# Kernel tuning notes

Hardware: AMD Instinct MI355X
Metric: run time of the kernel (lower is better)

Reference implementation:

```python
import jax, jax.numpy as jnp
import numpy as np

N_NODES = 50000
N_EDGES = 800000
N_GRAPHS = 2500
IN_DIM = 128
HID = 64
HEADS = 2
NEG_SLOPE = 0.2


def _gat_layer(x, W, att_src, att_dst, bias, src, dst, n):
    # W: [F_in, H*C], att_*: [H, C], bias: [C]
    h = (x @ W).reshape(n, HEADS, HID)            # [N,H,C]
    a_src = jnp.sum(h * att_src[None], axis=-1)   # [N,H]
    a_dst = jnp.sum(h * att_dst[None], axis=-1)   # [N,H]
    e = jax.nn.leaky_relu(a_src[src] + a_dst[dst], NEG_SLOPE)  # [E,H]
    # segment softmax over destination neighborhoods
    m = jax.ops.segment_max(e, dst, num_segments=n)            # [N,H]
    m = jnp.where(jnp.isfinite(m), m, 0.0)
    ex = jnp.exp(e - m[dst])
    s = jax.ops.segment_sum(ex, dst, num_segments=n)           # [N,H]
    alpha = ex / jnp.maximum(s[dst], 1e-16)                    # [E,H]
    msg = h[src] * alpha[:, :, None]                           # [E,H,C]
    out = jax.ops.segment_sum(msg, dst, num_segments=n)        # [N,H,C]
    return out.mean(axis=1) + bias                             # concat=False -> head mean


def _with_self_loops(edge_index, n):
    loop = jnp.arange(n, dtype=edge_index.dtype)
    src = jnp.concatenate([edge_index[0], loop])
    dst = jnp.concatenate([edge_index[1], loop])
    return src, dst


def setup_inputs() -> dict:
    key = jax.random.key(0)
    ks = jax.random.split(key, 16)
    x = jax.random.normal(ks[0], (N_NODES, IN_DIM), dtype=jnp.float32)
    edge_index = jax.random.randint(ks[1], (2, N_EDGES), 0, N_NODES, dtype=jnp.int32)
    batch = jnp.sort(jax.random.randint(ks[2], (N_NODES,), 0, N_GRAPHS, dtype=jnp.int32))

    def glorot(k, shape):
        fan = shape[0] + shape[-1]
        return jax.random.normal(k, shape, dtype=jnp.float32) * np.sqrt(2.0 / fan)

    inp = {"x": x, "edge_index": edge_index, "batch": batch}
    dims = [IN_DIM, HID, HID]
    for i in range(3):
        inp[f"W{i+1}"] = glorot(ks[3 + 4 * i], (dims[i], HEADS * HID))
        inp[f"att_src{i+1}"] = glorot(ks[4 + 4 * i], (HEADS, HID))
        inp[f"att_dst{i+1}"] = glorot(ks[5 + 4 * i], (HEADS, HID))
        inp[f"b{i+1}"] = jnp.zeros((HID,), dtype=jnp.float32)
    inp["lin_w"] = glorot(ks[15], (HID, 1))
    inp["lin_b"] = jnp.zeros((1,), dtype=jnp.float32)
    return inp


def reference(x, W1, att_src1, att_dst1, b1, W2, att_src2, att_dst2, b2,
              W3, att_src3, att_dst3, b3, lin_w, lin_b, edge_index, batch):
    n = x.shape[0]
    src, dst = _with_self_loops(edge_index, n)
    h = jax.nn.relu(_gat_layer(x, W1, att_src1, att_dst1, b1, src, dst, n))
    h = jax.nn.relu(_gat_layer(h, W2, att_src2, att_dst2, b2, src, dst, n))
    h = jax.nn.relu(_gat_layer(h, W3, att_src3, att_dst3, b3, src, dst, n))
    # global mean pool over graphs
    sums = jax.ops.segment_sum(h, batch, num_segments=N_GRAPHS)          # [G,C]
    cnt = jax.ops.segment_sum(jnp.ones((n,), h.dtype), batch, num_segments=N_GRAPHS)
    pooled = sums / jnp.maximum(cnt, 1.0)[:, None]
    return pooled @ lin_w + lin_b                                        # [G,1]
```

## Files before the change

### kernel.cpp

```cpp
#include <hip/hip_runtime.h>
#include <hip/hip_fp16.h>
#include <math.h>


__device__ __forceinline__ float lrelu(float v) { return v > 0.f ? v : 0.2f * v; }

__device__ __forceinline__ float wave_max(float v) {
  for (int off = 32; off; off >>= 1) v = fmaxf(v, __shfl_xor(v, off, 64));
  return v;
}
__device__ __forceinline__ float half_sum(float v) {
  for (int off = 16; off; off >>= 1) v += __shfl_xor(v, off, 64);
  return v;
}
__device__ __forceinline__ float half_max(float v) {
  for (int off = 16; off; off >>= 1) v = fmaxf(v, __shfl_xor(v, off, 64));
  return v;
}

__global__ void count_rank(const int* __restrict__ ei, int* __restrict__ deg,
                           int* __restrict__ rank, int e) {
  int j0 = blockIdx.x * 1024 + threadIdx.x;
#pragma unroll
  for (int k = 0; k < 4; ++k) {
    int j = j0 + k * 256;
    if (j < e) rank[j] = atomicAdd(&deg[ei[e + j]], 1);
  }
}

__global__ void scan_blocks(const int* __restrict__ deg, int* __restrict__ row_ptr,
                            int* __restrict__ btot, int n) {
  __shared__ int sm[256];
  int i = blockIdx.x * 256 + threadIdx.x;
  int v = (i < n) ? deg[i] : 0;
  sm[threadIdx.x] = v;
  __syncthreads();
  for (int off = 1; off < 256; off <<= 1) {
    int t = (threadIdx.x >= off) ? sm[threadIdx.x - off] : 0;
    __syncthreads();
    sm[threadIdx.x] += t;
    __syncthreads();
  }
  if (i < n) row_ptr[i] = sm[threadIdx.x] - v;
  if (threadIdx.x == 255) btot[blockIdx.x] = sm[255];
}

__global__ void scan_totals(int* __restrict__ btot, int nb) {
  __shared__ int sm[256];
  int v = (threadIdx.x < nb) ? btot[threadIdx.x] : 0;
  sm[threadIdx.x] = v;
  __syncthreads();
  for (int off = 1; off < 256; off <<= 1) {
    int t = (threadIdx.x >= off) ? sm[threadIdx.x - off] : 0;
    __syncthreads();
    sm[threadIdx.x] += t;
    __syncthreads();
  }
  if (threadIdx.x < nb) btot[threadIdx.x] = sm[threadIdx.x] - v;
}

__global__ void scan_add(int* __restrict__ row_ptr, int* __restrict__ csr,
                         const int* __restrict__ btot, int n, int total) {
  int i = blockIdx.x * 256 + threadIdx.x;
  if (i < n) {
    int v = row_ptr[i] + btot[blockIdx.x] + i;
    row_ptr[i] = v;
    csr[v] = i;
  }
  if (i == 0) row_ptr[n] = total;
}

__global__ void place_kernel(const int* __restrict__ ei, const int* __restrict__ rank,
                             const int* __restrict__ row_ptr, int* __restrict__ csr,
                             int e) {
  int j0 = blockIdx.x * 1024 + threadIdx.x;
#pragma unroll
  for (int k = 0; k < 4; ++k) {
    int j = j0 + k * 256;
    if (j < e) {
      int d = ei[e + j];
      csr[row_ptr[d] + 1 + rank[j]] = ei[j];
    }
  }
}

template <int K>
__global__ __launch_bounds__(256) void gemm_att(const float* __restrict__ X,
                                                const float* __restrict__ W,
                                                const float* __restrict__ asw,
                                                const float* __restrict__ adw,
                                                __half* __restrict__ H16,
                                                float* __restrict__ a_src,
                                                float* __restrict__ a_dst, int N) {
  __shared__ float Xs[64 * (K + 4)];
  int tid = threadIdx.x;
  int row0 = blockIdx.x * 64;
  int head = blockIdx.y;

  for (int idx = tid; idx < 64 * K; idx += 256) {
    int r = idx / K;
    int k = idx - r * K;
    int gr = row0 + r;
    if (gr >= N) gr = N - 1;
    Xs[r * (K + 4) + k] = X[(size_t)gr * K + k];
  }
  __syncthreads();

  int cgrp = tid & 15;
  int rg = tid >> 4;
  int c0 = head * 64 + cgrp * 4;
  const float* wp = W + c0;
  float acc[4][4] = {};

#pragma unroll 2
  for (int k = 0; k < K; k += 4) {
    float4 xr[4];
#pragma unroll
    for (int j = 0; j < 4; ++j)
      xr[j] = *(const float4*)(&Xs[(rg * 4 + j) * (K + 4) + k]);
#pragma unroll
    for (int kk = 0; kk < 4; ++kk) {
      float4 w4 = *(const float4*)(wp + (k + kk) * 128);
#pragma unroll
      for (int j = 0; j < 4; ++j) {
        float xv = ((const float*)&xr[j])[kk];
        acc[j][0] = fmaf(xv, w4.x, acc[j][0]);
        acc[j][1] = fmaf(xv, w4.y, acc[j][1]);
        acc[j][2] = fmaf(xv, w4.z, acc[j][2]);
        acc[j][3] = fmaf(xv, w4.w, acc[j][3]);
      }
    }
  }

  float4 aw = *(const float4*)(asw + c0);
  float4 dw = *(const float4*)(adw + c0);
#pragma unroll
  for (int j = 0; j < 4; ++j) {
    int r = row0 + rg * 4 + j;
    float sp = acc[j][0] * aw.x + acc[j][1] * aw.y + acc[j][2] * aw.z + acc[j][3] * aw.w;
    float dp = acc[j][0] * dw.x + acc[j][1] * dw.y + acc[j][2] * dw.z + acc[j][3] * dw.w;
#pragma unroll
    for (int off = 1; off < 16; off <<= 1) {
      sp += __shfl_xor(sp, off, 64);
      dp += __shfl_xor(dp, off, 64);
    }
    if (r < N) {
      union { __half2 h2[2]; uint2 u; } pk;
      pk.h2[0] = __floats2half2_rn(acc[j][0], acc[j][1]);
      pk.h2[1] = __floats2half2_rn(acc[j][2], acc[j][3]);
      *(uint2*)(H16 + (size_t)r * 128 + c0) = pk.u;
      if (cgrp == 0) {
        a_src[r * 2 + head] = sp;
        a_dst[r * 2 + head] = dp;
      }
    }
  }
}

__device__ __forceinline__ void ld_grp8(const __half* __restrict__ H16, int half_,
                                        int c8, int headsel, int sub, int s,
                                        float p0, float p1, int g,
                                        uint4* h, float* q) {
#pragma unroll
  for (int k = 0; k < 4; ++k) {
    int idx = half_ + g * 8 + k * 2 + sub;
    int st = __shfl(s, idx, 64);
    float q0 = __shfl(p0, idx, 64);
    float q1 = __shfl(p1, idx, 64);
    q[k] = headsel ? q1 : q0;
    h[k] = *(const uint4*)(H16 + (size_t)st * 128 + c8);
  }
}
__device__ __forceinline__ void fma_grp8(const uint4* h, const float* q,
                                         float* acc) {
#pragma unroll
  for (int k = 0; k < 4; ++k) {
    union { uint u; __half2 h2; } a, b, c, d;
    a.u = h[k].x; b.u = h[k].y; c.u = h[k].z; d.u = h[k].w;
    float2 f0 = __half22float2(a.h2);
    float2 f1 = __half22float2(b.h2);
    float2 f2 = __half22float2(c.h2);
    float2 f3 = __half22float2(d.h2);
    acc[0] = fmaf(f0.x, q[k], acc[0]);
    acc[1] = fmaf(f0.y, q[k], acc[1]);
    acc[2] = fmaf(f1.x, q[k], acc[2]);
    acc[3] = fmaf(f1.y, q[k], acc[3]);
    acc[4] = fmaf(f2.x, q[k], acc[4]);
    acc[5] = fmaf(f2.y, q[k], acc[5]);
    acc[6] = fmaf(f3.x, q[k], acc[6]);
    acc[7] = fmaf(f3.y, q[k], acc[7]);
  }
}
__device__ __forceinline__ void gather_pipe8(const __half* __restrict__ H16, int half_,
                                             int c8, int headsel, int sub, int s,
                                             float p0, float p1, int maxcnt,
                                             float* acc) {
  int groups = (maxcnt + 7) >> 3;
  uint4 ha[4], hb[4];
  float qa[4], qb[4];
  ld_grp8(H16, half_, c8, headsel, sub, s, p0, p1, 0, ha, qa);
  int g = 1;
  for (; g + 1 < groups; g += 2) {
    ld_grp8(H16, half_, c8, headsel, sub, s, p0, p1, g, hb, qb);
    fma_grp8(ha, qa, acc);
    ld_grp8(H16, half_, c8, headsel, sub, s, p0, p1, g + 1, ha, qa);
    fma_grp8(hb, qb, acc);
  }
  if (g < groups) {
    ld_grp8(H16, half_, c8, headsel, sub, s, p0, p1, g, hb, qb);
    fma_grp8(ha, qa, acc);
    fma_grp8(hb, qb, acc);
  } else {
    fma_grp8(ha, qa, acc);
  }
}

template <int POOL>
__global__ __launch_bounds__(256) void aggregate_fused(
    const __half* __restrict__ H16, const float* __restrict__ a_src,
    const float* __restrict__ a_dst, const float* __restrict__ bias,
    const int* __restrict__ row_ptr, const int* __restrict__ csr,
    float* __restrict__ out, const float* __restrict__ lw,
    float* __restrict__ pvn, int N) {
  int lane = threadIdx.x & 63;
  int half_ = lane & 32;
  int l32 = lane & 31;
  int dst = blockIdx.x * 8 + ((threadIdx.x >> 6) << 1) + (half_ >> 5);
  bool live = dst < N;
  int beg = live ? row_ptr[dst] : 0;
  int end = live ? row_ptr[dst + 1] : 0;
  int cnt = end - beg;
  float2 ad = live ? ((const float2*)a_dst)[dst] : make_float2(0.f, 0.f);
  int sub = l32 >> 4;
  int m = l32 & 15;
  int c8 = m * 8;
  int headsel = m >> 3;
  float acc[8] = {};
  float inv0, inv1;

  int maxcnt = (int)wave_max((float)cnt);
  if (maxcnt < 1) maxcnt = 1;

  if (maxcnt <= 32) {
    int j = beg + l32;
    bool valid = l32 < cnt;
    int s = valid ? csr[j] : 0;
    float2 as = ((const float2*)a_src)[s];
    float e0 = valid ? lrelu(as.x + ad.x) : -1e30f;
    float e1 = valid ? lrelu(as.y + ad.y) : -1e30f;
    float m0 = half_max(e0);
    float m1 = half_max(e1);
    float p0 = __expf(e0 - m0);
    float p1 = __expf(e1 - m1);
    inv0 = 1.f / fmaxf(half_sum(valid ? p0 : 0.f), 1e-16f);
    inv1 = 1.f / fmaxf(half_sum(valid ? p1 : 0.f), 1e-16f);
    gather_pipe8(H16, half_, c8, headsel, sub, s, p0, p1, maxcnt, acc);
  } else {
    float m0 = -1e30f, m1 = -1e30f, s0 = 0.f, s1 = 0.f;
    for (int base = 0; base < maxcnt; base += 32) {
      int j = beg + base + l32;
      bool valid = (base + l32) < cnt;
      int s = valid ? csr[j] : 0;
      float2 as = ((const float2*)a_src)[s];
      float e0 = valid ? lrelu(as.x + ad.x) : -1e30f;
      float e1 = valid ? lrelu(as.y + ad.y) : -1e30f;
      float nm0 = fmaxf(m0, half_max(e0));
      float nm1 = fmaxf(m1, half_max(e1));
      s0 = s0 * __expf(m0 - nm0) + half_sum(valid ? __expf(e0 - nm0) : 0.f);
      s1 = s1 * __expf(m1 - nm1) + half_sum(valid ? __expf(e1 - nm1) : 0.f);
      m0 = nm0; m1 = nm1;
    }
    inv0 = 1.f / fmaxf(s0, 1e-16f);
    inv1 = 1.f / fmaxf(s1, 1e-16f);
    for (int base = 0; base < maxcnt; base += 32) {
      int j = beg + base + l32;
      bool valid = (base + l32) < cnt;
      int s = valid ? csr[j] : 0;
      float2 as = ((const float2*)a_src)[s];
      float e0 = valid ? lrelu(as.x + ad.x) : -1e30f;
      float e1 = valid ? lrelu(as.y + ad.y) : -1e30f;
      float p0 = __expf(e0 - m0);
      float p1 = __expf(e1 - m1);
      int rem = maxcnt - base;
      if (rem > 32) rem = 32;
      gather_pipe8(H16, half_, c8, headsel, sub, s, p0, p1, rem, acc);
    }
  }

#pragma unroll
  for (int j = 0; j < 8; ++j) acc[j] += __shfl_xor(acc[j], 16, 64);

  float il = headsel ? inv1 : inv0;
  float v[8], w[8];
#pragma unroll
  for (int j = 0; j < 8; ++j) v[j] = acc[j] * il;
#pragma unroll
  for (int j = 0; j < 8; ++j) w[j] = __shfl_xor(v[j], 8, 64);

  if (m < 8 && sub == 0 && live) {
    int c = m * 8;
    float4 b0 = *(const float4*)(bias + c);
    float4 b1 = *(const float4*)(bias + c + 4);
    float r[8];
    r[0] = fmaxf(0.5f * (v[0] + w[0]) + b0.x, 0.f);
    r[1] = fmaxf(0.5f * (v[1] + w[1]) + b0.y, 0.f);
    r[2] = fmaxf(0.5f * (v[2] + w[2]) + b0.z, 0.f);
    r[3] = fmaxf(0.5f * (v[3] + w[3]) + b0.w, 0.f);
    r[4] = fmaxf(0.5f * (v[4] + w[4]) + b1.x, 0.f);
    r[5] = fmaxf(0.5f * (v[5] + w[5]) + b1.y, 0.f);
    r[6] = fmaxf(0.5f * (v[6] + w[6]) + b1.z, 0.f);
    r[7] = fmaxf(0.5f * (v[7] + w[7]) + b1.w, 0.f);
    if (POOL) {
      float4 l0 = *(const float4*)(lw + c);
      float4 l1 = *(const float4*)(lw + c + 4);
      float pv = r[0] * l0.x + r[1] * l0.y + r[2] * l0.z + r[3] * l0.w +
                 r[4] * l1.x + r[5] * l1.y + r[6] * l1.z + r[7] * l1.w;
      pv += __shfl_xor(pv, 1, 64);
      pv += __shfl_xor(pv, 2, 64);
      pv += __shfl_xor(pv, 4, 64);
      if (m == 0) pvn[dst] = pv;
    } else {
      *(float4*)(out + (size_t)dst * 64 + c) = make_float4(r[0], r[1], r[2], r[3]);
      *(float4*)(out + (size_t)dst * 64 + c + 4) = make_float4(r[4], r[5], r[6], r[7]);
    }
  }
}

__device__ __forceinline__ int lower_bound(const int* __restrict__ a, int n, int key) {
  int lo = 0, hi = n;
  while (lo < hi) {
    int mid = (lo + hi) >> 1;
    if (a[mid] < key) lo = mid + 1; else hi = mid;
  }
  return lo;
}

__global__ void finalize_kernel(const float* __restrict__ pvn,
                                const int* __restrict__ batch,
                                const float* __restrict__ lb,
                                float* __restrict__ out, int N, int G) {
  int g = blockIdx.x * blockDim.x + threadIdx.x;
  if (g >= G) return;
  int lo = lower_bound(batch, N, g);
  int hi = lower_bound(batch, N, g + 1);
  float s = 0.f;
  for (int i = lo; i < hi; ++i) s += pvn[i];
  out[g] = s / fmaxf((float)(hi - lo), 1.f) + lb[0];
}

extern "C" void kernel_launch(void* const* d_in, const int* in_sizes, int n_in,
                              void* d_out, int out_size, void* d_ws, size_t ws_size,
                              hipStream_t stream) {
  const float* x   = (const float*)d_in[0];
  const int* ei    = (const int*)d_in[1];
  const int* batch = (const int*)d_in[2];
  const float* W1  = (const float*)d_in[3];
  const float* as1 = (const float*)d_in[4];
  const float* ad1 = (const float*)d_in[5];
  const float* b1  = (const float*)d_in[6];
  const float* W2  = (const float*)d_in[7];
  const float* as2 = (const float*)d_in[8];
  const float* ad2 = (const float*)d_in[9];
  const float* b2  = (const float*)d_in[10];
  const float* W3  = (const float*)d_in[11];
  const float* as3 = (const float*)d_in[12];
  const float* ad3 = (const float*)d_in[13];
  const float* b3  = (const float*)d_in[14];
  const float* lw  = (const float*)d_in[15];
  const float* lb  = (const float*)d_in[16];
  float* out = (float*)d_out;

  const int N = in_sizes[0] / 128;
  const int E = in_sizes[1] / 2;
  const int ET = N + E;
  const int G = out_size;
  const int NB = (N + 255) / 256;

  char* p = (char*)d_ws;
  auto take = [&](size_t bytes) {
    char* r = p;
    p += (bytes + 255) & ~(size_t)255;
    return r;
  };
  int* deg      = (int*)take((size_t)N * 4);
  int* row_ptr  = (int*)take((size_t)(N + 1) * 4);
  int* rank     = (int*)take((size_t)E * 4);
  int* btot     = (int*)take((size_t)NB * 4);
  int* csr      = (int*)take((size_t)ET * 4);
  __half* H16   = (__half*)take((size_t)N * 128 * 2);
  float* a_src  = (float*)take((size_t)N * 2 * 4);
  float* a_dst  = (float*)take((size_t)N * 2 * 4);
  float* bufA   = (float*)take((size_t)N * 64 * 4);
  float* bufB   = (float*)take((size_t)N * 64 * 4);
  float* pvn    = (float*)take((size_t)N * 4);
  (void)ws_size; (void)n_in;

  hipMemsetAsync(deg, 0, (size_t)N * 4, stream);
  count_rank<<<(E + 1023) / 1024, 256, 0, stream>>>(ei, deg, rank, E);
  scan_blocks<<<NB, 256, 0, stream>>>(deg, row_ptr, btot, N);
  scan_totals<<<1, 256, 0, stream>>>(btot, NB);
  scan_add<<<NB, 256, 0, stream>>>(row_ptr, csr, btot, N, ET);
  place_kernel<<<(E + 1023) / 1024, 256, 0, stream>>>(ei, rank, row_ptr, csr, E);

  const dim3 gblk((N + 63) / 64, 2);
  const int ablk = (N + 7) / 8;

  gemm_att<128><<<gblk, 256, 0, stream>>>(x, W1, as1, ad1, H16, a_src, a_dst, N);
  aggregate_fused<0><<<ablk, 256, 0, stream>>>(H16, a_src, a_dst, b1, row_ptr, csr,
                                               bufA, lw, pvn, N);
  gemm_att<64><<<gblk, 256, 0, stream>>>(bufA, W2, as2, ad2, H16, a_src, a_dst, N);
  aggregate_fused<0><<<ablk, 256, 0, stream>>>(H16, a_src, a_dst, b2, row_ptr, csr,
                                               bufB, lw, pvn, N);
  gemm_att<64><<<gblk, 256, 0, stream>>>(bufB, W3, as3, ad3, H16, a_src, a_dst, N);
  aggregate_fused<1><<<ablk, 256, 0, stream>>>(H16, a_src, a_dst, b3, row_ptr, csr,
                                               bufA, lw, pvn, N);

  finalize_kernel<<<(G + 255) / 256, 256, 0, stream>>>(pvn, batch, lb, out, N, G);
}
```

Measured before the change: 348.4 us.

## Use one wavefront per destination node and K-chunk the GEMM shared tile

The aggregation kernel now maps each destination node to a full 64-lane wavefront instead of a half-wave, with four edge slots of 16 lanes each gathering rows in parallel, and uses wave-wide softmax reductions. This removes the per-wave maxcnt coupling between two nodes and gives more lanes per edge batch, but with about 17 edges per node most lanes are idle in the softmax phase and each wave does less work. Separately, the GEMM now stages X through a fixed 64-column shared tile in K chunks, reducing shared memory for K=128 at the cost of extra synchronisation.

```diff
diff --git a/kernel.cpp b/kernel.cpp
--- a/kernel.cpp
+++ b/kernel.cpp
@@ -9,12 +9,8 @@
   for (int off = 32; off; off >>= 1) v = fmaxf(v, __shfl_xor(v, off, 64));
   return v;
 }
-__device__ __forceinline__ float half_sum(float v) {
-  for (int off = 16; off; off >>= 1) v += __shfl_xor(v, off, 64);
-  return v;
-}
-__device__ __forceinline__ float half_max(float v) {
-  for (int off = 16; off; off >>= 1) v = fmaxf(v, __shfl_xor(v, off, 64));
+__device__ __forceinline__ float wave_sum(float v) {
+  for (int off = 32; off; off >>= 1) v += __shfl_xor(v, off, 64);
   return v;
 }
 
@@ -92,44 +88,46 @@
                                                 __half* __restrict__ H16,
                                                 float* __restrict__ a_src,
                                                 float* __restrict__ a_dst, int N) {
-  __shared__ float Xs[64 * (K + 4)];
+  __shared__ float Xs[64 * 68];
   int tid = threadIdx.x;
   int row0 = blockIdx.x * 64;
   int head = blockIdx.y;
-
-  for (int idx = tid; idx < 64 * K; idx += 256) {
-    int r = idx / K;
-    int k = idx - r * K;
-    int gr = row0 + r;
-    if (gr >= N) gr = N - 1;
-    Xs[r * (K + 4) + k] = X[(size_t)gr * K + k];
-  }
-  __syncthreads();
-
   int cgrp = tid & 15;
   int rg = tid >> 4;
   int c0 = head * 64 + cgrp * 4;
-  const float* wp = W + c0;
   float acc[4][4] = {};
 
+  for (int kc = 0; kc < K; kc += 64) {
+    for (int idx = tid; idx < 64 * 64; idx += 256) {
+      int r = idx >> 6;
+      int k = idx & 63;
+      int gr = row0 + r;
+      if (gr >= N) gr = N - 1;
+      Xs[r * 68 + k] = X[(size_t)gr * K + kc + k];
+    }
+    __syncthreads();
+
+    const float* wp = W + (size_t)kc * 128 + c0;
 #pragma unroll 2
-  for (int k = 0; k < K; k += 4) {
-    float4 xr[4];
-#pragma unroll
-    for (int j = 0; j < 4; ++j)
-      xr[j] = *(const float4*)(&Xs[(rg * 4 + j) * (K + 4) + k]);
-#pragma unroll
-    for (int kk = 0; kk < 4; ++kk) {
-      float4 w4 = *(const float4*)(wp + (k + kk) * 128);
-#pragma unroll
-      for (int j = 0; j < 4; ++j) {
-        float xv = ((const float*)&xr[j])[kk];
-        acc[j][0] = fmaf(xv, w4.x, acc[j][0]);
-        acc[j][1] = fmaf(xv, w4.y, acc[j][1]);
-        acc[j][2] = fmaf(xv, w4.z, acc[j][2]);
-        acc[j][3] = fmaf(xv, w4.w, acc[j][3]);
+    for (int k = 0; k < 64; k += 4) {
+      float4 xr[4];
+#pragma unroll
+      for (int j = 0; j < 4; ++j)
+        xr[j] = *(const float4*)(&Xs[(rg * 4 + j) * 68 + k]);
+#pragma unroll
+      for (int kk = 0; kk < 4; ++kk) {
+        float4 w4 = *(const float4*)(wp + (k + kk) * 128);
+#pragma unroll
+        for (int j = 0; j < 4; ++j) {
+          float xv = ((const float*)&xr[j])[kk];
+          acc[j][0] = fmaf(xv, w4.x, acc[j][0]);
+          acc[j][1] = fmaf(xv, w4.y, acc[j][1]);
+          acc[j][2] = fmaf(xv, w4.z, acc[j][2]);
+          acc[j][3] = fmaf(xv, w4.w, acc[j][3]);
+        }
       }
     }
+    __syncthreads();
   }
 
   float4 aw = *(const float4*)(asw + c0);
@@ -157,61 +155,61 @@
   }
 }
 
-__device__ __forceinline__ void ld_grp8(const __half* __restrict__ H16, int half_,
-                                        int c8, int headsel, int sub, int s,
+__device__ __forceinline__ void ld_grpw(const __half* __restrict__ H16, int q,
+                                        int c8, int headsel, int s,
                                         float p0, float p1, int g,
-                                        uint4* h, float* q) {
-#pragma unroll
-  for (int k = 0; k < 4; ++k) {
-    int idx = half_ + g * 8 + k * 2 + sub;
-    int st = __shfl(s, idx, 64);
-    float q0 = __shfl(p0, idx, 64);
-    float q1 = __shfl(p1, idx, 64);
-    q[k] = headsel ? q1 : q0;
+                                        uint4* h, float* qv) {
+#pragma unroll
+  for (int k = 0; k < 2; ++k) {
+    int e = g * 8 + k * 4 + q;
+    int st = __shfl(s, e, 64);
+    float q0 = __shfl(p0, e, 64);
+    float q1 = __shfl(p1, e, 64);
+    qv[k] = headsel ? q1 : q0;
     h[k] = *(const uint4*)(H16 + (size_t)st * 128 + c8);
   }
 }
-__device__ __forceinline__ void fma_grp8(const uint4* h, const float* q,
+__device__ __forceinline__ void fma_grpw(const uint4* h, const float* qv,
                                          float* acc) {
 #pragma unroll
-  for (int k = 0; k < 4; ++k) {
+  for (int k = 0; k < 2; ++k) {
     union { uint u; __half2 h2; } a, b, c, d;
     a.u = h[k].x; b.u = h[k].y; c.u = h[k].z; d.u = h[k].w;
     float2 f0 = __half22float2(a.h2);
     float2 f1 = __half22float2(b.h2);
     float2 f2 = __half22float2(c.h2);
     float2 f3 = __half22float2(d.h2);
-    acc[0] = fmaf(f0.x, q[k], acc[0]);
-    acc[1] = fmaf(f0.y, q[k], acc[1]);
-    acc[2] = fmaf(f1.x, q[k], acc[2]);
-    acc[3] = fmaf(f1.y, q[k], acc[3]);
-    acc[4] = fmaf(f2.x, q[k], acc[4]);
-    acc[5] = fmaf(f2.y, q[k], acc[5]);
-    acc[6] = fmaf(f3.x, q[k], acc[6]);
-    acc[7] = fmaf(f3.y, q[k], acc[7]);
-  }
-}
-__device__ __forceinline__ void gather_pipe8(const __half* __restrict__ H16, int half_,
-                                             int c8, int headsel, int sub, int s,
+    acc[0] = fmaf(f0.x, qv[k], acc[0]);
+    acc[1] = fmaf(f0.y, qv[k], acc[1]);
+    acc[2] = fmaf(f1.x, qv[k], acc[2]);
+    acc[3] = fmaf(f1.y, qv[k], acc[3]);
+    acc[4] = fmaf(f2.x, qv[k], acc[4]);
+    acc[5] = fmaf(f2.y, qv[k], acc[5]);
+    acc[6] = fmaf(f3.x, qv[k], acc[6]);
+    acc[7] = fmaf(f3.y, qv[k], acc[7]);
+  }
+}
+__device__ __forceinline__ void gather_pipew(const __half* __restrict__ H16, int q,
+                                             int c8, int headsel, int s,
                                              float p0, float p1, int maxcnt,
                                              float* acc) {
   int groups = (maxcnt + 7) >> 3;
-  uint4 ha[4], hb[4];
-  float qa[4], qb[4];
-  ld_grp8(H16, half_, c8, headsel, sub, s, p0, p1, 0, ha, qa);
+  uint4 ha[2], hb[2];
+  float qa[2], qb[2];
+  ld_grpw(H16, q, c8, headsel, s, p0, p1, 0, ha, qa);
   int g = 1;
   for (; g + 1 < groups; g += 2) {
-    ld_grp8(H16, half_, c8, headsel, sub, s, p0, p1, g, hb, qb);
-    fma_grp8(ha, qa, acc);
-    ld_grp8(H16, half_, c8, headsel, sub, s, p0, p1, g + 1, ha, qa);
-    fma_grp8(hb, qb, acc);
+    ld_grpw(H16, q, c8, headsel, s, p0, p1, g, hb, qb);
+    fma_grpw(ha, qa, acc);
+    ld_grpw(H16, q, c8, headsel, s, p0, p1, g + 1, ha, qa);
+    fma_grpw(hb, qb, acc);
   }
   if (g < groups) {
-    ld_grp8(H16, half_, c8, headsel, sub, s, p0, p1, g, hb, qb);
-    fma_grp8(ha, qa, acc);
-    fma_grp8(hb, qb, acc);
+    ld_grpw(H16, q, c8, headsel, s, p0, p1, g, hb, qb);
+    fma_grpw(ha, qa, acc);
+    fma_grpw(hb, qb, acc);
   } else {
-    fma_grp8(ha, qa, acc);
+    fma_grpw(ha, qa, acc);
   }
 }
 
@@ -222,73 +220,70 @@
     const int* __restrict__ row_ptr, const int* __restrict__ csr,
     float* __restrict__ out, const float* __restrict__ lw,
     float* __restrict__ pvn, int N) {
+  int dst = blockIdx.x * 4 + (threadIdx.x >> 6);
+  if (dst >= N) return;
   int lane = threadIdx.x & 63;
-  int half_ = lane & 32;
-  int l32 = lane & 31;
-  int dst = blockIdx.x * 8 + ((threadIdx.x >> 6) << 1) + (half_ >> 5);
-  bool live = dst < N;
-  int beg = live ? row_ptr[dst] : 0;
-  int end = live ? row_ptr[dst + 1] : 0;
-  int cnt = end - beg;
-  float2 ad = live ? ((const float2*)a_dst)[dst] : make_float2(0.f, 0.f);
-  int sub = l32 >> 4;
-  int m = l32 & 15;
+  int q = lane >> 4;
+  int m = lane & 15;
   int c8 = m * 8;
   int headsel = m >> 3;
+  int beg = row_ptr[dst], end = row_ptr[dst + 1];
+  int cnt = end - beg;
+  float2 ad = ((const float2*)a_dst)[dst];
   float acc[8] = {};
   float inv0, inv1;
 
-  int maxcnt = (int)wave_max((float)cnt);
-  if (maxcnt < 1) maxcnt = 1;
-
-  if (maxcnt <= 32) {
-    int j = beg + l32;
-    bool valid = l32 < cnt;
+  if (cnt <= 64) {
+    int j = beg + lane;
+    bool valid = lane < cnt;
     int s = valid ? csr[j] : 0;
     float2 as = ((const float2*)a_src)[s];
     float e0 = valid ? lrelu(as.x + ad.x) : -1e30f;
     float e1 = valid ? lrelu(as.y + ad.y) : -1e30f;
-    float m0 = half_max(e0);
-    float m1 = half_max(e1);
+    float m0 = wave_max(e0);
+    float m1 = wave_max(e1);
     float p0 = __expf(e0 - m0);
     float p1 = __expf(e1 - m1);
-    inv0 = 1.f / fmaxf(half_sum(valid ? p0 : 0.f), 1e-16f);
-    inv1 = 1.f / fmaxf(half_sum(valid ? p1 : 0.f), 1e-16f);
-    gather_pipe8(H16, half_, c8, headsel, sub, s, p0, p1, maxcnt, acc);
+    inv0 = 1.f / fmaxf(wave_sum(valid ? p0 : 0.f), 1e-16f);
+    inv1 = 1.f / fmaxf(wave_sum(valid ? p1 : 0.f), 1e-16f);
+    gather_pipew(H16, q, c8, headsel, s, p0, p1, cnt, acc);
   } else {
     float m0 = -1e30f, m1 = -1e30f, s0 = 0.f, s1 = 0.f;
-    for (int base = 0; base < maxcnt; base += 32) {
-      int j = beg + base + l32;
-      bool valid = (base + l32) < cnt;
+    for (int base = 0; base < cnt; base += 64) {
+      int j = beg + base + lane;
+      bool valid = (base + lane) < cnt;
       int s = valid ? csr[j] : 0;
       float2 as = ((const float2*)a_src)[s];
       float e0 = valid ? lrelu(as.x + ad.x) : -1e30f;
       float e1 = valid ? lrelu(as.y + ad.y) : -1e30f;
-      float nm0 = fmaxf(m0, half_max(e0));
-      float nm1 = fmaxf(m1, half_max(e1));
-      s0 = s0 * __expf(m0 - nm0) + half_sum(valid ? __expf(e0 - nm0) : 0.f);
-      s1 = s1 * __expf(m1 - nm1) + half_sum(valid ? __expf(e1 - nm1) : 0.f);
+      float nm0 = fmaxf(m0, wave_max(e0));
+      float nm1 = fmaxf(m1, wave_max(e1));
+      s0 = s0 * __expf(m0 - nm0) + wave_sum(valid ? __expf(e0 - nm0) : 0.f);
+      s1 = s1 * __expf(m1 - nm1) + wave_sum(valid ? __expf(e1 - nm1) : 0.f);
       m0 = nm0; m1 = nm1;
     }
     inv0 = 1.f / fmaxf(s0, 1e-16f);
     inv1 = 1.f / fmaxf(s1, 1e-16f);
-    for (int base = 0; base < maxcnt; base += 32) {
-      int j = beg + base + l32;
-      bool valid = (base + l32) < cnt;
+    for (int base = 0; base < cnt; base += 64) {
+      int j = beg + base + lane;
+      bool valid = (base + lane) < cnt;
       int s = valid ? csr[j] : 0;
       float2 as = ((const float2*)a_src)[s];
       float e0 = valid ? lrelu(as.x + ad.x) : -1e30f;
       float e1 = valid ? lrelu(as.y + ad.y) : -1e30f;
       float p0 = __expf(e0 - m0);
       float p1 = __expf(e1 - m1);
-      int rem = maxcnt - base;
-      if (rem > 32) rem = 32;
-      gather_pipe8(H16, half_, c8, headsel, sub, s, p0, p1, rem, acc);
-    }
-  }
-
-#pragma unroll
-  for (int j = 0; j < 8; ++j) acc[j] += __shfl_xor(acc[j], 16, 64);
+      int rem = cnt - base;
+      if (rem > 64) rem = 64;
+      gather_pipew(H16, q, c8, headsel, s, p0, p1, rem, acc);
+    }
+  }
+
+#pragma unroll
+  for (int j = 0; j < 8; ++j) {
+    acc[j] += __shfl_xor(acc[j], 16, 64);
+    acc[j] += __shfl_xor(acc[j], 32, 64);
+  }
 
   float il = headsel ? inv1 : inv0;
   float v[8], w[8];
@@ -297,8 +292,8 @@
 #pragma unroll
   for (int j = 0; j < 8; ++j) w[j] = __shfl_xor(v[j], 8, 64);
 
-  if (m < 8 && sub == 0 && live) {
-    int c = m * 8;
+  if (lane < 8) {
+    int c = lane * 8;
     float4 b0 = *(const float4*)(bias + c);
     float4 b1 = *(const float4*)(bias + c + 4);
     float r[8];
@@ -318,7 +313,7 @@
       pv += __shfl_xor(pv, 1, 64);
       pv += __shfl_xor(pv, 2, 64);
       pv += __shfl_xor(pv, 4, 64);
-      if (m == 0) pvn[dst] = pv;
+      if (lane == 0) pvn[dst] = pv;
     } else {
       *(float4*)(out + (size_t)dst * 64 + c) = make_float4(r[0], r[1], r[2], r[3]);
       *(float4*)(out + (size_t)dst * 64 + c + 4) = make_float4(r[4], r[5], r[6], r[7]);
@@ -403,7 +398,7 @@
   place_kernel<<<(E + 1023) / 1024, 256, 0, stream>>>(ei, rank, row_ptr, csr, E);
 
   const dim3 gblk((N + 63) / 64, 2);
-  const int ablk = (N + 7) / 8;
+  const int ablk = (N + 3) / 4;
 
   gemm_att<128><<<gblk, 256, 0, stream>>>(x, W1, as1, ad1, H16, a_src, a_dst, N);
   aggregate_fused<0><<<ablk, 256, 0, stream>>>(H16, a_src, a_dst, b1, row_ptr, csr,
```

After: 358.7 us. 1.03x slower.
